# Kernel tuning notes

Measured on AMD Instinct MI355X. Metric: run time of the kernel, lower is better.

## Reference

```python
import jax, jax.numpy as jnp
import numpy as np

N = 50000      # nodes
E = 1600000    # edges per graph
IN = 64
HID = 64
OUT = 64


def _gat_conv(x, edge_index, W, a_src, a_dst, bias):
    """PyG GATConv, heads=1, add_self_loops=True, negative_slope=0.2."""
    n = x.shape[0]
    h = x @ W                                   # [N, d]
    loop = jnp.arange(n, dtype=edge_index.dtype)
    src = jnp.concatenate([edge_index[0], loop])
    dst = jnp.concatenate([edge_index[1], loop])
    e = jax.nn.leaky_relu((h @ a_src)[src] + (h @ a_dst)[dst], negative_slope=0.2)
    m = jax.ops.segment_max(e, dst, num_segments=n)          # stable edge-softmax per dst
    w = jnp.exp(e - m[dst])
    denom = jax.ops.segment_sum(w, dst, num_segments=n)
    alpha = w / denom[dst]                                   # [E+N]
    out = jax.ops.segment_sum(h[src] * alpha[:, None], dst, num_segments=n)
    return out + bias


def setup_inputs() -> dict:
    key = jax.random.key(0)
    ks = jax.random.split(key, 32)

    def glorot(k, shape):
        fan_out = shape[1] if len(shape) > 1 else 1
        lim = (6.0 / (shape[0] + fan_out)) ** 0.5
        return jax.random.uniform(k, shape, minval=-lim, maxval=lim, dtype=jnp.float32)

    inp = {
        "x_ind": jax.random.normal(ks[0], (N, IN), jnp.float32),
        "x_pos": jax.random.normal(ks[1], (N, IN), jnp.float32),
        "edge_ind": jax.random.randint(ks[2], (2, E), 0, N, dtype=jnp.int32),
        "edge_pos": jax.random.randint(ks[3], (2, E), 0, N, dtype=jnp.int32),
        "w1_ind": glorot(ks[4], (IN, HID)),
        "as1_ind": glorot(ks[5], (HID,)),
        "ad1_ind": glorot(ks[6], (HID,)),
        "b1_ind": jnp.zeros((HID,), jnp.float32),
        "w2_ind": glorot(ks[7], (HID, OUT)),
        "as2_ind": glorot(ks[8], (OUT,)),
        "ad2_ind": glorot(ks[9], (OUT,)),
        "b2_ind": jnp.zeros((OUT,), jnp.float32),
        "w1_pos": glorot(ks[10], (IN, HID)),
        "as1_pos": glorot(ks[11], (HID,)),
        "ad1_pos": glorot(ks[12], (HID,)),
        "b1_pos": jnp.zeros((HID,), jnp.float32),
        "w2_pos": glorot(ks[13], (HID, OUT)),
        "as2_pos": glorot(ks[14], (OUT,)),
        "ad2_pos": glorot(ks[15], (OUT,)),
        "b2_pos": jnp.zeros((OUT,), jnp.float32),
        "first_hop_att": glorot(ks[16], (2, HID)),
        "att_weight": glorot(ks[17], (2, OUT)),
        "mlp_w": glorot(ks[18], (OUT, 1)),
        "mlp_b": jnp.zeros((1,), jnp.float32),
    }
    return inp


def reference(x_ind, x_pos, edge_ind, edge_pos,
              w1_ind, as1_ind, ad1_ind, b1_ind,
              w2_ind, as2_ind, ad2_ind, b2_ind,
              w1_pos, as1_pos, ad1_pos, b1_pos,
              w2_pos, as2_pos, ad2_pos, b2_pos,
              first_hop_att, att_weight, mlp_w, mlp_b):
    h_i = jax.nn.relu(_gat_conv(x_ind, edge_ind, w1_ind, as1_ind, ad1_ind, b1_ind))
    h_p = jax.nn.relu(_gat_conv(x_pos, edge_pos, w1_pos, as1_pos, ad1_pos, b1_pos))
    # first-hop branch attention over the two graphs
    s1 = jnp.stack([jnp.sum(first_hop_att[0] * h_i, axis=1),
                    jnp.sum(first_hop_att[1] * h_p, axis=1)], axis=0)  # [2, N]
    a1 = jax.nn.softmax(s1, axis=0)
    fused = a1[0][:, None] * h_i + a1[1][:, None] * h_p
    g_i = _gat_conv(fused, edge_ind, w2_ind, as2_ind, ad2_ind, b2_ind)
    g_p = _gat_conv(fused, edge_pos, w2_pos, as2_pos, ad2_pos, b2_pos)
    s2 = jnp.stack([jnp.sum(att_weight[0] * g_i, axis=1),
                    jnp.sum(att_weight[1] * g_p, axis=1)], axis=0)
    a2 = jax.nn.softmax(s2, axis=0)
    x = a2[0][:, None] * g_i + a2[1][:, None] * g_p
    return x @ mlp_w + mlp_b                    # [N, 1]
```

## Files before the change

### kernel.cpp

```cpp
#include <hip/hip_runtime.h>
#include <hip/hip_fp16.h>

#define ND 64
#define BG 128
#define MAXB 1024
#define PCH 16384
#define CAP 4608

__device__ __forceinline__ float lrelu(float x) { return x > 0.f ? x : 0.2f * x; }

__device__ __forceinline__ float wave_sum(float v) {
#pragma unroll
    for (int m = 32; m > 0; m >>= 1) v += __shfl_xor(v, m, 64);
    return v;
}

__device__ __forceinline__ void fma8(float* acc, float w, int4 raw) {
    union { int4 i; __half h[8]; } u;
    u.i = raw;
#pragma unroll
    for (int i = 0; i < 8; i++) acc[i] = fmaf(w, __half2float(u.h[i]), acc[i]);
}


__global__ void init_cursor(int* __restrict__ bcursor, int nb) {
    int t = threadIdx.x;
    if (t < nb) bcursor[t] = t * CAP;
}

__device__ void partition_body(int* hist, int* lcur,
                               const int* __restrict__ eI, const int* __restrict__ eP,
                               int* __restrict__ bcursor, int* __restrict__ part,
                               int N, int E, int nb) {
    int t = threadIdx.x;
    int total = 2 * E;
    int chunkBase = blockIdx.x * PCH;
    int cnt = min(PCH, total - chunkBase);
    if (t < nb) hist[t] = 0;
    __syncthreads();

    if (cnt == PCH) {
        int pk[16];
        unsigned bkp[8];
#pragma unroll
        for (int it = 0; it < 4; it++) {
            int i = t * 4 + it * 4096;
            int e = chunkBase + i;
            int sv[4], dv[4];
            if (e + 3 < E) {
                int4 a = *(const int4*)(eI + e);
                int4 b = *(const int4*)(eI + E + e);
                sv[0] = a.x; sv[1] = a.y; sv[2] = a.z; sv[3] = a.w;
                dv[0] = b.x; dv[1] = b.y; dv[2] = b.z; dv[3] = b.w;
            } else if (e >= E) {
                int4 a = *(const int4*)(eP + (e - E));
                int4 b = *(const int4*)(eP + E + (e - E));
                sv[0] = a.x; sv[1] = a.y; sv[2] = a.z; sv[3] = a.w;
                dv[0] = b.x + N; dv[1] = b.y + N; dv[2] = b.z + N; dv[3] = b.w + N;
            } else {
#pragma unroll
                for (int k = 0; k < 4; k++) {
                    int ee = e + k;
                    if (ee < E) { sv[k] = eI[ee]; dv[k] = eI[E + ee]; }
                    else        { sv[k] = eP[ee - E]; dv[k] = N + eP[E + ee - E]; }
                }
            }
#pragma unroll
            for (int k = 0; k < 4; k++) {
                int j = it * 4 + k;
                int bk = dv[k] >> 7;
                pk[j] = (sv[k] << 8) | (dv[k] & 255);
                atomicAdd(&hist[bk], 1);
                if ((j & 1) == 0) bkp[j >> 1] = (unsigned)bk;
                else bkp[j >> 1] |= (unsigned)bk << 16;
            }
        }
        __syncthreads();
        if (t < nb) lcur[t] = hist[t] ? atomicAdd(&bcursor[t], hist[t]) : 0;
        __syncthreads();
#pragma unroll
        for (int j = 0; j < 16; j++) {
            int bk = (bkp[j >> 1] >> ((j & 1) * 16)) & 0xffff;
            int pos = atomicAdd(&lcur[bk], 1);
            part[pos] = pk[j];
        }
        return;
    }

    int cnt4 = cnt & ~3;
    for (int i = t * 4; i < cnt4; i += 4096) {
        int e = chunkBase + i;
        int4 d; int base;
        if (e + 3 < E)   { d = *(const int4*)(eI + E + e); base = 0; }
        else if (e >= E) { d = *(const int4*)(eP + E + (e - E)); base = N; }
        else {
            int tmp[4];
#pragma unroll
            for (int k = 0; k < 4; k++) {
                int ee = e + k;
                tmp[k] = (ee < E) ? eI[E + ee] : N + eP[E + ee - E];
            }
            d = make_int4(tmp[0], tmp[1], tmp[2], tmp[3]); base = 0;
        }
        atomicAdd(&hist[(base + d.x) >> 7], 1);
        atomicAdd(&hist[(base + d.y) >> 7], 1);
        atomicAdd(&hist[(base + d.z) >> 7], 1);
        atomicAdd(&hist[(base + d.w) >> 7], 1);
    }
    for (int i = cnt4 + t; i < cnt; i += 1024) {
        int e = chunkBase + i;
        int idx = (e < E) ? eI[E + e] : N + eP[E + (e - E)];
        atomicAdd(&hist[idx >> 7], 1);
    }
    __syncthreads();
    if (t < nb) lcur[t] = hist[t] ? atomicAdd(&bcursor[t], hist[t]) : 0;
    __syncthreads();
    for (int i = t; i < cnt; i += 1024) {
        int e = chunkBase + i;
        int s, idx;
        if (e < E) { s = eI[e]; idx = eI[E + e]; }
        else       { s = eP[e - E]; idx = N + eP[E + (e - E)]; }
        int pos = atomicAdd(&lcur[idx >> 7], 1);
        part[pos] = (s << 8) | (idx & 255);
    }
}

__device__ void gemm_body(float* xsAll, int gb,
                          const float* __restrict__ xA, const float* __restrict__ xB,
                          const float* __restrict__ WA, const float* __restrict__ WB,
                          const float* __restrict__ asA, const float* __restrict__ adA,
                          const float* __restrict__ asB, const float* __restrict__ adB,
                          __half* __restrict__ h16, float* __restrict__ ssrc,
                          float* __restrict__ sdst, int N) {
    int half = gb & 1;
    int blk = gb >> 1;
    int wave = threadIdx.x >> 6;
    int lane = threadIdx.x & 63;
    const float* x  = half ? xB : xA;
    const float* W  = half ? WB : WA;
    const float* av_ = half ? asB : asA;
    const float* dv_ = half ? adB : adA;
    int nodeBase = (blk * 16 + wave) * 4;
    float* xs = xsAll + wave * (4 * ND);

    if (nodeBase + 3 < N) {
        *(float4*)&xs[lane * 4] = *(const float4*)&x[(size_t)nodeBase * ND + lane * 4];
    } else if (nodeBase < N) {
#pragma unroll
        for (int i = 0; i < 4; i++) {
            int gi = nodeBase * ND + lane * 4 + i;
            xs[lane * 4 + i] = (gi < N * ND) ? x[gi] : 0.f;
        }
    }
    __syncthreads();
    if (nodeBase >= N) return;

    float4 acc = {0.f, 0.f, 0.f, 0.f};
#pragma unroll
    for (int k = 0; k < ND; k++) {
        float wv = W[k * ND + lane];
        acc.x = fmaf(xs[0 * ND + k], wv, acc.x);
        acc.y = fmaf(xs[1 * ND + k], wv, acc.y);
        acc.z = fmaf(xs[2 * ND + k], wv, acc.z);
        acc.w = fmaf(xs[3 * ND + k], wv, acc.w);
    }
    float av = av_[lane], dv = dv_[lane];
    float s1x = wave_sum(acc.x * av), s2x = wave_sum(acc.x * dv);
    float s1y = wave_sum(acc.y * av), s2y = wave_sum(acc.y * dv);
    float s1z = wave_sum(acc.z * av), s2z = wave_sum(acc.z * dv);
    float s1w = wave_sum(acc.w * av), s2w = wave_sum(acc.w * dv);

    int g0 = half * N + nodeBase;
    h16[(size_t)(g0 + 0) * ND + lane] = __float2half(acc.x);
    if (nodeBase + 1 < N) h16[(size_t)(g0 + 1) * ND + lane] = __float2half(acc.y);
    if (nodeBase + 2 < N) h16[(size_t)(g0 + 2) * ND + lane] = __float2half(acc.z);
    if (nodeBase + 3 < N) h16[(size_t)(g0 + 3) * ND + lane] = __float2half(acc.w);
    if (lane == 0) {
        ssrc[g0] = s1x; sdst[g0] = s2x;
        if (nodeBase + 1 < N) { ssrc[g0 + 1] = s1y; sdst[g0 + 1] = s2y; }
        if (nodeBase + 2 < N) { ssrc[g0 + 2] = s1z; sdst[g0 + 2] = s2z; }
        if (nodeBase + 3 < N) { ssrc[g0 + 3] = s1w; sdst[g0 + 3] = s2w; }
    }
}

__global__ void __launch_bounds__(1024) part_gemm(
        const int* __restrict__ eI, const int* __restrict__ eP,
        int* __restrict__ bcursor, int* __restrict__ part,
        const float* __restrict__ xA, const float* __restrict__ xB,
        const float* __restrict__ WA, const float* __restrict__ WB,
        const float* __restrict__ asA, const float* __restrict__ adA,
        const float* __restrict__ asB, const float* __restrict__ adB,
        __half* __restrict__ h16, float* __restrict__ ssrc, float* __restrict__ sdst,
        int N, int E, int nb, int partBlocks) {
    __shared__ int smem[16 * 4 * ND];
    if (blockIdx.x < partBlocks) {
        partition_body(smem, smem + MAXB, eI, eP, bcursor, part, N, E, nb);
    } else {
        gemm_body((float*)smem, blockIdx.x - partBlocks,
                  xA, xB, WA, WB, asA, adA, asB, adB, h16, ssrc, sdst, N);
    }
}

__global__ void bucket_build(const int* __restrict__ part, const int* __restrict__ bcursor,
                             int* __restrict__ row, int* __restrict__ deg,
                             int* __restrict__ csr, int n2, int N) {
    __shared__ int lhist[BG * 8];
    __shared__ int lrow[BG * 8];
    __shared__ int slab[CAP];
    int b = blockIdx.x, t = threadIdx.x;
    int start = b * CAP;
    int cnt = min(bcursor[b] - start, CAP);
    int cnt4 = cnt & ~3;
    int t1 = (N * 1) >> 3, t2 = (N * 2) >> 3, t3 = (N * 3) >> 3, t4 = (N * 4) >> 3;
    int t5 = (N * 5) >> 3, t6 = (N * 6) >> 3, t7 = (N * 7) >> 3;
    auto key = [&](int p) {
        int s = p >> 8;
        int o = (s >= t1) + (s >= t2) + (s >= t3) + (s >= t4)
              + (s >= t5) + (s >= t6) + (s >= t7);
        return ((p & 127) << 3) | o;
    };
    lhist[t] = 0;
    __syncthreads();
    for (int j = t * 4; j < cnt4; j += 4096) {
        int4 p = *(const int4*)(part + start + j);
        atomicAdd(&lhist[key(p.x)], 1);
        atomicAdd(&lhist[key(p.y)], 1);
        atomicAdd(&lhist[key(p.z)], 1);
        atomicAdd(&lhist[key(p.w)], 1);
    }
    for (int j = cnt4 + t; j < cnt; j += 1024) atomicAdd(&lhist[key(part[start + j])], 1);
    __syncthreads();
    int v = lhist[t];
    lrow[t] = v;
    __syncthreads();
    for (int off = 1; off < 1024; off <<= 1) {
        int a = (t >= off) ? lrow[t - off] : 0;
        __syncthreads();
        lrow[t] += a;
        __syncthreads();
    }
    if (t < BG) {
        int g = b * BG + t;
        if (g < n2) {
            row[g] = start + lrow[8 * t] - lhist[8 * t];
            int d = 0;
#pragma unroll
            for (int i = 0; i < 8; i++) d += lhist[8 * t + i];
            deg[g] = d;
        }
    }
    __syncthreads();
    lhist[t] = lrow[t] - v;
    __syncthreads();
    for (int j = t * 4; j < cnt4; j += 4096) {
        int4 p = *(const int4*)(part + start + j);
        int pos;
        pos = atomicAdd(&lhist[key(p.x)], 1); slab[pos] = p.x >> 8;
        pos = atomicAdd(&lhist[key(p.y)], 1); slab[pos] = p.y >> 8;
        pos = atomicAdd(&lhist[key(p.z)], 1); slab[pos] = p.z >> 8;
        pos = atomicAdd(&lhist[key(p.w)], 1); slab[pos] = p.w >> 8;
    }
    for (int j = cnt4 + t; j < cnt; j += 1024) {
        int p = part[start + j];
        int pos = atomicAdd(&lhist[key(p)], 1);
        slab[pos] = p >> 8;
    }
    __syncthreads();
    {
        int ge = lrow[t], gs = ge - v;
        for (int i = gs + 1; i < ge; i++) {
            int x = slab[i], j2 = i - 1;
            while (j2 >= gs && slab[j2] > x) { slab[j2 + 1] = slab[j2]; j2--; }
            slab[j2 + 1] = x;
        }
    }
    __syncthreads();
    for (int j = t; j < cnt; j += 1024) csr[start + j] = slab[j];
}

__global__ void gemm2_fused(const float* __restrict__ hbig, const float* __restrict__ fha,
                            const float* __restrict__ WA, const float* __restrict__ WB,
                            const float* __restrict__ asA, const float* __restrict__ adA,
                            const float* __restrict__ asB, const float* __restrict__ adB,
                            __half* __restrict__ h16, float* __restrict__ ssrc,
                            float* __restrict__ sdst, int N) {
    __shared__ float xs[4][4 * ND];
    int half = blockIdx.x & 1;
    int blk = blockIdx.x >> 1;
    int wave = threadIdx.x >> 6;
    int lane = threadIdx.x & 63;
    const float* W  = half ? WB : WA;
    const float* av_ = half ? asB : asA;
    const float* dv_ = half ? adB : adA;
    int nodeBase = (blk * 4 + wave) * 4;
    float* xsw = xs[wave];

    if (nodeBase < N) {
        int nd = nodeBase + (lane >> 4);
        int col = (lane & 15) * 4;
        float4 vi = *(const float4*)&hbig[(size_t)nd * ND + col];
        float4 vp = *(const float4*)&hbig[((size_t)N + nd) * ND + col];
        float4 a0 = *(const float4*)&fha[col];
        float4 a1 = *(const float4*)&fha[ND + col];
        float p0 = vi.x * a0.x + vi.y * a0.y + vi.z * a0.z + vi.w * a0.w;
        float p1 = vp.x * a1.x + vp.y * a1.y + vp.z * a1.z + vp.w * a1.w;
#pragma unroll
        for (int m = 1; m <= 8; m <<= 1) {
            p0 += __shfl_xor(p0, m, 64);
            p1 += __shfl_xor(p1, m, 64);
        }
        float mx = fmaxf(p0, p1);
        float e0 = __expf(p0 - mx), e1 = __expf(p1 - mx);
        float inv = 1.f / (e0 + e1);
        float4 f;
        f.x = (e0 * vi.x + e1 * vp.x) * inv;
        f.y = (e0 * vi.y + e1 * vp.y) * inv;
        f.z = (e0 * vi.z + e1 * vp.z) * inv;
        f.w = (e0 * vi.w + e1 * vp.w) * inv;
        *(float4*)&xsw[lane * 4] = f;
    }
    __syncthreads();
    if (nodeBase >= N) return;

    float4 acc = {0.f, 0.f, 0.f, 0.f};
#pragma unroll
    for (int k = 0; k < ND; k++) {
        float wv = W[k * ND + lane];
        acc.x = fmaf(xsw[0 * ND + k], wv, acc.x);
        acc.y = fmaf(xsw[1 * ND + k], wv, acc.y);
        acc.z = fmaf(xsw[2 * ND + k], wv, acc.z);
        acc.w = fmaf(xsw[3 * ND + k], wv, acc.w);
    }
    float av = av_[lane], dv = dv_[lane];
    float s1x = wave_sum(acc.x * av), s2x = wave_sum(acc.x * dv);
    float s1y = wave_sum(acc.y * av), s2y = wave_sum(acc.y * dv);
    float s1z = wave_sum(acc.z * av), s2z = wave_sum(acc.z * dv);
    float s1w = wave_sum(acc.w * av), s2w = wave_sum(acc.w * dv);

    int g0 = half * N + nodeBase;
    h16[(size_t)(g0 + 0) * ND + lane] = __float2half(acc.x);
    h16[(size_t)(g0 + 1) * ND + lane] = __float2half(acc.y);
    h16[(size_t)(g0 + 2) * ND + lane] = __float2half(acc.z);
    h16[(size_t)(g0 + 3) * ND + lane] = __float2half(acc.w);
    if (lane == 0) {
        ssrc[g0] = s1x; sdst[g0] = s2x;
        ssrc[g0 + 1] = s1y; sdst[g0 + 1] = s2y;
        ssrc[g0 + 2] = s1z; sdst[g0 + 2] = s2z;
        ssrc[g0 + 3] = s1w; sdst[g0 + 3] = s2w;
    }
}

__global__ void aggregate_dual(const int* __restrict__ csr, const int* __restrict__ row,
                               const int* __restrict__ deg, const float* __restrict__ ssrc,
                               const float* __restrict__ sdst, const __half* __restrict__ h16,
                               const float* __restrict__ bA, const float* __restrict__ bB,
                               float* __restrict__ out, int N, int relu) {
    int half = blockIdx.x & 1;
    int wave = threadIdx.x >> 6;
    int lane = threadIdx.x & 63;
    int sub  = lane >> 4;
    int l16  = lane & 15;
    int slot = l16 >> 3;
    int fl8  = (l16 & 7) * 8;
    int node = ((blockIdx.x >> 1) * 4 + wave) * 4 + sub;
    bool valid = node < N;
    int g = half * N + node;
    const float* bias = half ? bB : bA;
    const float* ss = ssrc + (size_t)half * N;
    const __half* hh = h16 + (size_t)half * N * ND;
    const char* hp = (const char*)hh;
    int flb = fl8 * 2;

    int start = valid ? row[g] : 0;
    int cnt   = valid ? deg[g] : 0;
    float sd  = valid ? sdst[g] : 0.f;
    float wself = valid ? __expf(lrelu(ss[node] + sd)) : 0.f;

    float acc[8] = {0.f, 0.f, 0.f, 0.f, 0.f, 0.f, 0.f, 0.f};
    float denomp = 0.f;
    int lbase = (sub << 4) + slot;

    int c16 = min(16, cnt);
    int sj = (l16 < c16) ? csr[start + l16] : 0;
    float wj = (l16 < c16) ? __expf(lrelu(ss[sj] + sd)) : 0.f;

    for (int base = 0; base < cnt; base += 16) {
        int nb2 = base + 16;
        int sn = 0; float vn = 0.f; int cn = cnt - nb2;
        if (nb2 < cnt) {
            sn = (l16 < cn) ? csr[start + nb2 + l16] : 0;
            vn = (l16 < cn) ? ss[sn] : 0.f;
        }
        denomp += wj;
        int sjb = sj << 7;
#pragma unroll
        for (int c = 0; c < 8; c++) {
            float w = __shfl(wj, lbase + 2 * c, 64);
            int   o = __shfl(sjb, lbase + 2 * c, 64);
            int4 r = *(const int4*)(hp + (o | flb));
            fma8(acc, w, r);
        }
        if (nb2 < cnt) {
            wj = (l16 < cn) ? __expf(lrelu(vn + sd)) : 0.f;
            sj = sn;
        }
    }

#pragma unroll
    for (int i = 0; i < 8; i++) acc[i] += __shfl_xor(acc[i], 8, 64);
#pragma unroll
    for (int m = 1; m <= 8; m <<= 1) denomp += __shfl_xor(denomp, m, 64);
    float denom = denomp + wself;

    if (!valid || slot != 0) return;
    int4 rawS = *(const int4*)(hh + (size_t)node * ND + fl8);
    union { int4 i; __half h[8]; } us;
    us.i = rawS;
    float v[8];
#pragma unroll
    for (int i = 0; i < 8; i++)
        v[i] = (acc[i] + wself * __half2float(us.h[i])) / denom + bias[fl8 + i];
    if (relu) {
#pragma unroll
        for (int i = 0; i < 8; i++) v[i] = fmaxf(v[i], 0.f);
    }
    *(float4*)&out[(size_t)g * ND + fl8]     = make_float4(v[0], v[1], v[2], v[3]);
    *(float4*)&out[(size_t)g * ND + fl8 + 4] = make_float4(v[4], v[5], v[6], v[7]);
}

__global__ void branch_att_mlp(const float* __restrict__ hbig, const float* __restrict__ att,
                               const float* __restrict__ mlpw, const float* __restrict__ mlpb,
                               float* __restrict__ out, int n) {
    int gid = blockIdx.x * blockDim.x + threadIdx.x;
    int node = gid >> 6, lane = gid & 63;
    if (node >= n) return;
    float vi = hbig[(size_t)node * ND + lane];
    float vp = hbig[((size_t)n + node) * ND + lane];
    float s0 = wave_sum(att[lane] * vi);
    float s1 = wave_sum(att[ND + lane] * vp);
    float m = fmaxf(s0, s1);
    float a0 = __expf(s0 - m), a1 = __expf(s1 - m);
    float xj = (a0 * vi + a1 * vp) / (a0 + a1);
    float o = wave_sum(xj * mlpw[lane]);
    if (lane == 0) out[node] = o + mlpb[0];
}

extern "C" void kernel_launch(void* const* d_in, const int* in_sizes, int n_in,
                              void* d_out, int out_size, void* d_ws, size_t ws_size,
                              hipStream_t stream) {
    const int N = in_sizes[0] / ND;
    const int E = in_sizes[2] / 2;

    const float* x_ind = (const float*)d_in[0];
    const float* x_pos = (const float*)d_in[1];
    const int*   e_ind = (const int*)d_in[2];
    const int*   e_pos = (const int*)d_in[3];
    const float* w1i = (const float*)d_in[4];
    const float* as1i = (const float*)d_in[5];
    const float* ad1i = (const float*)d_in[6];
    const float* b1i = (const float*)d_in[7];
    const float* w2i = (const float*)d_in[8];
    const float* as2i = (const float*)d_in[9];
    const float* ad2i = (const float*)d_in[10];
    const float* b2i = (const float*)d_in[11];
    const float* w1p = (const float*)d_in[12];
    const float* as1p = (const float*)d_in[13];
    const float* ad1p = (const float*)d_in[14];
    const float* b1p = (const float*)d_in[15];
    const float* w2p = (const float*)d_in[16];
    const float* as2p = (const float*)d_in[17];
    const float* ad2p = (const float*)d_in[18];
    const float* b2p = (const float*)d_in[19];
    const float* fha = (const float*)d_in[20];
    const float* attw = (const float*)d_in[21];
    const float* mlpw = (const float*)d_in[22];
    const float* mlpb = (const float*)d_in[23];

    char* ws = (char*)d_ws;
    size_t off = 0;
    auto alloc = [&](size_t elems) { void* p = ws + off; off += elems * 4; return p; };

    const int n2 = 2 * N;
    const int nb = (n2 + BG - 1) / BG;

    __half* h16 = (__half*)alloc((size_t)n2 * ND / 2);
    float* hbig = (float*)alloc((size_t)n2 * ND);
    float* ssrc = (float*)alloc(n2);
    float* sdst = (float*)alloc(n2);
    int* deg    = (int*)alloc(n2);
    int* rowi   = (int*)alloc(n2);
    int* csr    = (int*)alloc((size_t)nb * CAP);
    int* bcursor= (int*)alloc(MAXB);
    int* part   = (int*)hbig;

    const int partBlocks  = (2 * E + PCH - 1) / PCH;
    const int gemm1Blocks = 2 * ((N + 63) / 64);
    const int gemm2Blocks = 2 * ((N + 15) / 16);
    const int aggBlocks   = 2 * ((N + 15) / 16);
    const int nodeBlocks  = (N + 3) / 4;

    init_cursor<<<1, 1024, 0, stream>>>(bcursor, nb);
    part_gemm<<<partBlocks + gemm1Blocks, 1024, 0, stream>>>(
        e_ind, e_pos, bcursor, part,
        x_ind, x_pos, w1i, w1p, as1i, ad1i, as1p, ad1p,
        h16, ssrc, sdst, N, E, nb, partBlocks);
    bucket_build<<<nb, 1024, 0, stream>>>(part, bcursor, rowi, deg, csr, n2, N);

    aggregate_dual<<<aggBlocks, 256, 0, stream>>>(csr, rowi, deg, ssrc, sdst, h16,
                                                  b1i, b1p, hbig, N, 1);

    gemm2_fused<<<gemm2Blocks, 256, 0, stream>>>(hbig, fha, w2i, w2p,
                                                 as2i, ad2i, as2p, ad2p,
                                                 h16, ssrc, sdst, N);
    aggregate_dual<<<aggBlocks, 256, 0, stream>>>(csr, rowi, deg, ssrc, sdst, h16,
                                                  b2i, b2p, hbig, N, 0);
    branch_att_mlp<<<nodeBlocks, 256, 0, stream>>>(hbig, attw, mlpw, mlpb,
                                                   (float*)d_out, N);
}
```

Measured before the change: 337.9 us.

## Fuse aggregation with branch attention and GEMM2, and with final MLP

Merges the first aggregation with branch attention and the second-layer GEMM, and the second aggregation with branch attention and the MLP head. Each block now handles 8 nodes for both graphs and keeps the intermediate features in LDS. This removes the fp32 hbig round trips and two kernel launches. The gather loop is also rewritten with a software-pipelined, variable-length chain that skips empty slots instead of always issuing 8 loads. In exchange, block-level syncs now tie together the two graphs' aggregation waves, so load imbalance between their degrees can stall a block.

```diff
diff --git a/kernel.cpp b/kernel.cpp
--- a/kernel.cpp
+++ b/kernel.cpp
@@ -278,133 +278,183 @@
     for (int j = t; j < cnt; j += 1024) csr[start + j] = slab[j];
 }
 
-__global__ void gemm2_fused(const float* __restrict__ hbig, const float* __restrict__ fha,
-                            const float* __restrict__ WA, const float* __restrict__ WB,
-                            const float* __restrict__ asA, const float* __restrict__ adA,
-                            const float* __restrict__ asB, const float* __restrict__ adB,
-                            __half* __restrict__ h16, float* __restrict__ ssrc,
-                            float* __restrict__ sdst, int N) {
-    __shared__ float xs[4][4 * ND];
-    int half = blockIdx.x & 1;
-    int blk = blockIdx.x >> 1;
-    int wave = threadIdx.x >> 6;
-    int lane = threadIdx.x & 63;
-    const float* W  = half ? WB : WA;
-    const float* av_ = half ? asB : asA;
-    const float* dv_ = half ? adB : adA;
-    int nodeBase = (blk * 4 + wave) * 4;
-    float* xsw = xs[wave];
-
-    if (nodeBase < N) {
-        int nd = nodeBase + (lane >> 4);
-        int col = (lane & 15) * 4;
-        float4 vi = *(const float4*)&hbig[(size_t)nd * ND + col];
-        float4 vp = *(const float4*)&hbig[((size_t)N + nd) * ND + col];
-        float4 a0 = *(const float4*)&fha[col];
-        float4 a1 = *(const float4*)&fha[ND + col];
-        float p0 = vi.x * a0.x + vi.y * a0.y + vi.z * a0.z + vi.w * a0.w;
-        float p1 = vp.x * a1.x + vp.y * a1.y + vp.z * a1.z + vp.w * a1.w;
-#pragma unroll
-        for (int m = 1; m <= 8; m <<= 1) {
-            p0 += __shfl_xor(p0, m, 64);
-            p1 += __shfl_xor(p1, m, 64);
-        }
+
+__device__ __forceinline__ void gather_body(
+        const int* __restrict__ csr, int start, int cnt, float sd,
+        const float* __restrict__ ss, const __half* __restrict__ hh,
+        int l16, int slot, int fl8, int waveBase,
+        float* acc, float& denomp) {
+    int c16 = min(16, cnt);
+    int sj = (l16 < c16) ? csr[start + l16] : 0;
+    float wj = (l16 < c16) ? __expf(lrelu(ss[sj] + sd)) : 0.f;
+
+    for (int base = 0; base < cnt; base += 16) {
+        int nb2 = base + 16;
+        int sjn = 0; float svn = 0.f; int c16n = cnt - nb2;
+        if (nb2 < cnt) {
+            sjn = (l16 < c16n) ? csr[start + nb2 + l16] : 0;
+            svn = (l16 < c16n) ? ss[sjn] : 0.f;
+        }
+        denomp += wj;
+        int nq = (min(16, cnt - base) + 1) >> 1;
+        float w0 = __shfl(wj, waveBase + slot, 64);
+        int s0 = __shfl(sj, waveBase + slot, 64);
+        int4 r0 = *(const int4*)(hh + (size_t)s0 * ND + fl8);
+        if (nq > 1) {
+            float w1 = __shfl(wj, waveBase + 2 + slot, 64);
+            int s1 = __shfl(sj, waveBase + 2 + slot, 64);
+            int4 r1 = *(const int4*)(hh + (size_t)s1 * ND + fl8);
+            for (int c = 2; c < nq; c++) {
+                float w2 = __shfl(wj, waveBase + c * 2 + slot, 64);
+                int s2 = __shfl(sj, waveBase + c * 2 + slot, 64);
+                int4 r2 = *(const int4*)(hh + (size_t)s2 * ND + fl8);
+                fma8(acc, w0, r0);
+                w0 = w1; r0 = r1;
+                w1 = w2; r1 = r2;
+            }
+            fma8(acc, w0, r0);
+            fma8(acc, w1, r1);
+        } else {
+            fma8(acc, w0, r0);
+        }
+        if (nb2 < cnt) {
+            wj = (l16 < c16n) ? __expf(lrelu(svn + sd)) : 0.f;
+            sj = sjn;
+        }
+    }
+}
+
+__global__ void agg1_gemm2(
+        const int* __restrict__ csr, const int* __restrict__ row,
+        const int* __restrict__ deg, const float* __restrict__ ss1,
+        const float* __restrict__ sd1, const __half* __restrict__ h16a,
+        const float* __restrict__ b1A, const float* __restrict__ b1B,
+        const float* __restrict__ fha,
+        const float* __restrict__ W2A, const float* __restrict__ W2B,
+        const float* __restrict__ as2A, const float* __restrict__ ad2A,
+        const float* __restrict__ as2B, const float* __restrict__ ad2B,
+        __half* __restrict__ h16b, float* __restrict__ ssrc2,
+        float* __restrict__ sdst2, int N) {
+    __shared__ float lds_h[2][8][ND];
+    __shared__ float lds_f[8][ND];
+    int wave = threadIdx.x >> 6, lane = threadIdx.x & 63;
+    int half = wave >> 1;
+    int sub = lane >> 4, l16 = lane & 15, slot = l16 >> 3, fl8 = (l16 & 7) * 8;
+    int nodeIdx = (wave & 1) * 4 + sub;
+    int node = blockIdx.x * 8 + nodeIdx;
+    bool valid = node < N;
+    int g = half * N + node;
+    const float* bias = half ? b1B : b1A;
+    const float* ss = ss1 + (size_t)half * N;
+    const __half* hh = h16a + (size_t)half * N * ND;
+
+    int start = valid ? row[g] : 0;
+    int cnt   = valid ? deg[g] : 0;
+    float sd  = valid ? sd1[g] : 0.f;
+    float wself = valid ? __expf(lrelu(ss[node] + sd)) : 0.f;
+
+    float acc[8] = {0.f, 0.f, 0.f, 0.f, 0.f, 0.f, 0.f, 0.f};
+    float denomp = 0.f;
+    gather_body(csr, start, cnt, sd, ss, hh, l16, slot, fl8, sub << 4, acc, denomp);
+
+#pragma unroll
+    for (int i = 0; i < 8; i++) acc[i] += __shfl_xor(acc[i], 8, 64);
+#pragma unroll
+    for (int m = 1; m <= 8; m <<= 1) denomp += __shfl_xor(denomp, m, 64);
+    float denom = denomp + wself;
+
+    if (slot == 0) {
+        if (valid) {
+            int4 rawS = *(const int4*)(hh + (size_t)node * ND + fl8);
+            union { int4 i; __half h[8]; } us;
+            us.i = rawS;
+#pragma unroll
+            for (int i = 0; i < 8; i++)
+                lds_h[half][nodeIdx][fl8 + i] =
+                    fmaxf((acc[i] + wself * __half2float(us.h[i])) / denom + bias[fl8 + i], 0.f);
+        } else {
+#pragma unroll
+            for (int i = 0; i < 8; i++) lds_h[half][nodeIdx][fl8 + i] = 0.f;
+        }
+    }
+    __syncthreads();
+
+#pragma unroll
+    for (int r = 0; r < 2; r++) {
+        int n = wave * 2 + r;
+        float vi = lds_h[0][n][lane], vp = lds_h[1][n][lane];
+        float p0 = wave_sum(fha[lane] * vi);
+        float p1 = wave_sum(fha[ND + lane] * vp);
         float mx = fmaxf(p0, p1);
         float e0 = __expf(p0 - mx), e1 = __expf(p1 - mx);
         float inv = 1.f / (e0 + e1);
-        float4 f;
-        f.x = (e0 * vi.x + e1 * vp.x) * inv;
-        f.y = (e0 * vi.y + e1 * vp.y) * inv;
-        f.z = (e0 * vi.z + e1 * vp.z) * inv;
-        f.w = (e0 * vi.w + e1 * vp.w) * inv;
-        *(float4*)&xsw[lane * 4] = f;
-    }
-    __syncthreads();
-    if (nodeBase >= N) return;
-
-    float4 acc = {0.f, 0.f, 0.f, 0.f};
-#pragma unroll
-    for (int k = 0; k < ND; k++) {
-        float wv = W[k * ND + lane];
-        acc.x = fmaf(xsw[0 * ND + k], wv, acc.x);
-        acc.y = fmaf(xsw[1 * ND + k], wv, acc.y);
-        acc.z = fmaf(xsw[2 * ND + k], wv, acc.z);
-        acc.w = fmaf(xsw[3 * ND + k], wv, acc.w);
-    }
-    float av = av_[lane], dv = dv_[lane];
-    float s1x = wave_sum(acc.x * av), s2x = wave_sum(acc.x * dv);
-    float s1y = wave_sum(acc.y * av), s2y = wave_sum(acc.y * dv);
-    float s1z = wave_sum(acc.z * av), s2z = wave_sum(acc.z * dv);
-    float s1w = wave_sum(acc.w * av), s2w = wave_sum(acc.w * dv);
-
-    int g0 = half * N + nodeBase;
-    h16[(size_t)(g0 + 0) * ND + lane] = __float2half(acc.x);
-    h16[(size_t)(g0 + 1) * ND + lane] = __float2half(acc.y);
-    h16[(size_t)(g0 + 2) * ND + lane] = __float2half(acc.z);
-    h16[(size_t)(g0 + 3) * ND + lane] = __float2half(acc.w);
-    if (lane == 0) {
-        ssrc[g0] = s1x; sdst[g0] = s2x;
-        ssrc[g0 + 1] = s1y; sdst[g0 + 1] = s2y;
-        ssrc[g0 + 2] = s1z; sdst[g0 + 2] = s2z;
-        ssrc[g0 + 3] = s1w; sdst[g0 + 3] = s2w;
-    }
-}
-
-__global__ void aggregate_dual(const int* __restrict__ csr, const int* __restrict__ row,
-                               const int* __restrict__ deg, const float* __restrict__ ssrc,
-                               const float* __restrict__ sdst, const __half* __restrict__ h16,
-                               const float* __restrict__ bA, const float* __restrict__ bB,
-                               float* __restrict__ out, int N, int relu) {
-    int half = blockIdx.x & 1;
-    int wave = threadIdx.x >> 6;
-    int lane = threadIdx.x & 63;
-    int sub  = lane >> 4;
-    int l16  = lane & 15;
-    int slot = l16 >> 3;
-    int fl8  = (l16 & 7) * 8;
-    int node = ((blockIdx.x >> 1) * 4 + wave) * 4 + sub;
+        lds_f[n][lane] = (e0 * vi + e1 * vp) * inv;
+    }
+    __syncthreads();
+
+    {
+        const float* W  = half ? W2B : W2A;
+        const float* av_ = half ? as2B : as2A;
+        const float* dv_ = half ? ad2B : ad2A;
+        int nb0 = (wave & 1) * 4;
+        float4 a2 = {0.f, 0.f, 0.f, 0.f};
+#pragma unroll
+        for (int k = 0; k < ND; k++) {
+            float wv = W[k * ND + lane];
+            a2.x = fmaf(lds_f[nb0 + 0][k], wv, a2.x);
+            a2.y = fmaf(lds_f[nb0 + 1][k], wv, a2.y);
+            a2.z = fmaf(lds_f[nb0 + 2][k], wv, a2.z);
+            a2.w = fmaf(lds_f[nb0 + 3][k], wv, a2.w);
+        }
+        float av = av_[lane], dv = dv_[lane];
+        float s1x = wave_sum(a2.x * av), s2x = wave_sum(a2.x * dv);
+        float s1y = wave_sum(a2.y * av), s2y = wave_sum(a2.y * dv);
+        float s1z = wave_sum(a2.z * av), s2z = wave_sum(a2.z * dv);
+        float s1w = wave_sum(a2.w * av), s2w = wave_sum(a2.w * dv);
+
+        int n0 = blockIdx.x * 8 + nb0;
+        int g0 = half * N + n0;
+        if (n0 + 0 < N) h16b[(size_t)(g0 + 0) * ND + lane] = __float2half(a2.x);
+        if (n0 + 1 < N) h16b[(size_t)(g0 + 1) * ND + lane] = __float2half(a2.y);
+        if (n0 + 2 < N) h16b[(size_t)(g0 + 2) * ND + lane] = __float2half(a2.z);
+        if (n0 + 3 < N) h16b[(size_t)(g0 + 3) * ND + lane] = __float2half(a2.w);
+        if (lane == 0) {
+            if (n0 + 0 < N) { ssrc2[g0 + 0] = s1x; sdst2[g0 + 0] = s2x; }
+            if (n0 + 1 < N) { ssrc2[g0 + 1] = s1y; sdst2[g0 + 1] = s2y; }
+            if (n0 + 2 < N) { ssrc2[g0 + 2] = s1z; sdst2[g0 + 2] = s2z; }
+            if (n0 + 3 < N) { ssrc2[g0 + 3] = s1w; sdst2[g0 + 3] = s2w; }
+        }
+    }
+}
+
+__global__ void agg2_mlp(
+        const int* __restrict__ csr, const int* __restrict__ row,
+        const int* __restrict__ deg, const float* __restrict__ ss2,
+        const float* __restrict__ sd2, const __half* __restrict__ h16b,
+        const float* __restrict__ b2A, const float* __restrict__ b2B,
+        const float* __restrict__ attw, const float* __restrict__ mlpw,
+        const float* __restrict__ mlpb,
+        float* __restrict__ out, int N) {
+    __shared__ float lds_h[2][8][ND];
+    int wave = threadIdx.x >> 6, lane = threadIdx.x & 63;
+    int half = wave >> 1;
+    int sub = lane >> 4, l16 = lane & 15, slot = l16 >> 3, fl8 = (l16 & 7) * 8;
+    int nodeIdx = (wave & 1) * 4 + sub;
+    int node = blockIdx.x * 8 + nodeIdx;
     bool valid = node < N;
     int g = half * N + node;
-    const float* bias = half ? bB : bA;
-    const float* ss = ssrc + (size_t)half * N;
-    const __half* hh = h16 + (size_t)half * N * ND;
-    const char* hp = (const char*)hh;
-    int flb = fl8 * 2;
+    const float* bias = half ? b2B : b2A;
+    const float* ss = ss2 + (size_t)half * N;
+    const __half* hh = h16b + (size_t)half * N * ND;
 
     int start = valid ? row[g] : 0;
     int cnt   = valid ? deg[g] : 0;
-    float sd  = valid ? sdst[g] : 0.f;
+    float sd  = valid ? sd2[g] : 0.f;
     float wself = valid ? __expf(lrelu(ss[node] + sd)) : 0.f;
 
     float acc[8] = {0.f, 0.f, 0.f, 0.f, 0.f, 0.f, 0.f, 0.f};
     float denomp = 0.f;
-    int lbase = (sub << 4) + slot;
-
-    int c16 = min(16, cnt);
-    int sj = (l16 < c16) ? csr[start + l16] : 0;
-    float wj = (l16 < c16) ? __expf(lrelu(ss[sj] + sd)) : 0.f;
-
-    for (int base = 0; base < cnt; base += 16) {
-        int nb2 = base + 16;
-        int sn = 0; float vn = 0.f; int cn = cnt - nb2;
-        if (nb2 < cnt) {
-            sn = (l16 < cn) ? csr[start + nb2 + l16] : 0;
-            vn = (l16 < cn) ? ss[sn] : 0.f;
-        }
-        denomp += wj;
-        int sjb = sj << 7;
-#pragma unroll
-        for (int c = 0; c < 8; c++) {
-            float w = __shfl(wj, lbase + 2 * c, 64);
-            int   o = __shfl(sjb, lbase + 2 * c, 64);
-            int4 r = *(const int4*)(hp + (o | flb));
-            fma8(acc, w, r);
-        }
-        if (nb2 < cnt) {
-            wj = (l16 < cn) ? __expf(lrelu(vn + sd)) : 0.f;
-            sj = sn;
-        }
-    }
+    gather_body(csr, start, cnt, sd, ss, hh, l16, slot, fl8, sub << 4, acc, denomp);
 
 #pragma unroll
     for (int i = 0; i < 8; i++) acc[i] += __shfl_xor(acc[i], 8, 64);
@@ -412,37 +462,35 @@
     for (int m = 1; m <= 8; m <<= 1) denomp += __shfl_xor(denomp, m, 64);
     float denom = denomp + wself;
 
-    if (!valid || slot != 0) return;
-    int4 rawS = *(const int4*)(hh + (size_t)node * ND + fl8);
-    union { int4 i; __half h[8]; } us;
-    us.i = rawS;
-    float v[8];
-#pragma unroll
-    for (int i = 0; i < 8; i++)
-        v[i] = (acc[i] + wself * __half2float(us.h[i])) / denom + bias[fl8 + i];
-    if (relu) {
-#pragma unroll
-        for (int i = 0; i < 8; i++) v[i] = fmaxf(v[i], 0.f);
-    }
-    *(float4*)&out[(size_t)g * ND + fl8]     = make_float4(v[0], v[1], v[2], v[3]);
-    *(float4*)&out[(size_t)g * ND + fl8 + 4] = make_float4(v[4], v[5], v[6], v[7]);
-}
-
-__global__ void branch_att_mlp(const float* __restrict__ hbig, const float* __restrict__ att,
-                               const float* __restrict__ mlpw, const float* __restrict__ mlpb,
-                               float* __restrict__ out, int n) {
-    int gid = blockIdx.x * blockDim.x + threadIdx.x;
-    int node = gid >> 6, lane = gid & 63;
-    if (node >= n) return;
-    float vi = hbig[(size_t)node * ND + lane];
-    float vp = hbig[((size_t)n + node) * ND + lane];
-    float s0 = wave_sum(att[lane] * vi);
-    float s1 = wave_sum(att[ND + lane] * vp);
-    float m = fmaxf(s0, s1);
-    float a0 = __expf(s0 - m), a1 = __expf(s1 - m);
-    float xj = (a0 * vi + a1 * vp) / (a0 + a1);
-    float o = wave_sum(xj * mlpw[lane]);
-    if (lane == 0) out[node] = o + mlpb[0];
+    if (slot == 0) {
+        if (valid) {
+            int4 rawS = *(const int4*)(hh + (size_t)node * ND + fl8);
+            union { int4 i; __half h[8]; } us;
+            us.i = rawS;
+#pragma unroll
+            for (int i = 0; i < 8; i++)
+                lds_h[half][nodeIdx][fl8 + i] =
+                    (acc[i] + wself * __half2float(us.h[i])) / denom + bias[fl8 + i];
+        } else {
+#pragma unroll
+            for (int i = 0; i < 8; i++) lds_h[half][nodeIdx][fl8 + i] = 0.f;
+        }
+    }
+    __syncthreads();
+
+#pragma unroll
+    for (int r = 0; r < 2; r++) {
+        int n = wave * 2 + r;
+        int gn = blockIdx.x * 8 + n;
+        float vi = lds_h[0][n][lane], vp = lds_h[1][n][lane];
+        float s0 = wave_sum(attw[lane] * vi);
+        float s1 = wave_sum(attw[ND + lane] * vp);
+        float m = fmaxf(s0, s1);
+        float a0 = __expf(s0 - m), a1 = __expf(s1 - m);
+        float xj = (a0 * vi + a1 * vp) / (a0 + a1);
+        float o = wave_sum(xj * mlpw[lane]);
+        if (lane == 0 && gn < N) out[gn] = o + mlpb[0];
+    }
 }
 
 extern "C" void kernel_launch(void* const* d_in, const int* in_sizes, int n_in,
@@ -483,37 +531,34 @@
     const int n2 = 2 * N;
     const int nb = (n2 + BG - 1) / BG;
 
-    __half* h16 = (__half*)alloc((size_t)n2 * ND / 2);
-    float* hbig = (float*)alloc((size_t)n2 * ND);
-    float* ssrc = (float*)alloc(n2);
-    float* sdst = (float*)alloc(n2);
+    __half* h16a = (__half*)alloc((size_t)n2 * ND / 2);
+    float* ssrc1 = (float*)alloc(n2);
+    float* sdst1 = (float*)alloc(n2);
+    float* ssrc2 = (float*)alloc(n2);
+    float* sdst2 = (float*)alloc(n2);
     int* deg    = (int*)alloc(n2);
     int* rowi   = (int*)alloc(n2);
     int* csr    = (int*)alloc((size_t)nb * CAP);
     int* bcursor= (int*)alloc(MAXB);
-    int* part   = (int*)hbig;
+    int* part   = (int*)alloc((size_t)nb * CAP);
+    __half* h16b = (__half*)part;
 
     const int partBlocks  = (2 * E + PCH - 1) / PCH;
     const int gemm1Blocks = 2 * ((N + 63) / 64);
-    const int gemm2Blocks = 2 * ((N + 15) / 16);
-    const int aggBlocks   = 2 * ((N + 15) / 16);
-    const int nodeBlocks  = (N + 3) / 4;
+    const int fusedBlocks = (N + 7) / 8;
 
     init_cursor<<<1, 1024, 0, stream>>>(bcursor, nb);
     part_gemm<<<partBlocks + gemm1Blocks, 1024, 0, stream>>>(
         e_ind, e_pos, bcursor, part,
         x_ind, x_pos, w1i, w1p, as1i, ad1i, as1p, ad1p,
-        h16, ssrc, sdst, N, E, nb, partBlocks);
+        h16a, ssrc1, sdst1, N, E, nb, partBlocks);
     bucket_build<<<nb, 1024, 0, stream>>>(part, bcursor, rowi, deg, csr, n2, N);
 
-    aggregate_dual<<<aggBlocks, 256, 0, stream>>>(csr, rowi, deg, ssrc, sdst, h16,
-                                                  b1i, b1p, hbig, N, 1);
-
-    gemm2_fused<<<gemm2Blocks, 256, 0, stream>>>(hbig, fha, w2i, w2p,
-                                                 as2i, ad2i, as2p, ad2p,
-                                                 h16, ssrc, sdst, N);
-    aggregate_dual<<<aggBlocks, 256, 0, stream>>>(csr, rowi, deg, ssrc, sdst, h16,
-                                                  b2i, b2p, hbig, N, 0);
-    branch_att_mlp<<<nodeBlocks, 256, 0, stream>>>(hbig, attw, mlpw, mlpb,
-                                                   (float*)d_out, N);
-}
+    agg1_gemm2<<<fusedBlocks, 256, 0, stream>>>(
+        csr, rowi, deg, ssrc1, sdst1, h16a, b1i, b1p, fha,
+        w2i, w2p, as2i, ad2i, as2p, ad2p, h16b, ssrc2, sdst2, N);
+
+    agg2_mlp<<<fusedBlocks, 256, 0, stream>>>(
+        csr, rowi, deg, ssrc2, sdst2, h16b, b2i, b2p,
+        attw, mlpw, mlpb, (float*)d_out, N);
+}
```

New measurement: 333.9 us. About the same (-1.2%).
